# Performance work log

Measured on AMD Instinct MI355X. Metric: run time of the kernel, lower is better.

Reference implementation:

```python
import jax, jax.numpy as jnp
import numpy as np

MAX_LV = 2
N_NODES = 20000
N_CLASSES = 16


def setup_inputs() -> dict:
    key = jax.random.key(0)
    ks = jax.random.split(key, 20)
    B, E, A, F, D, H, NI = 8, 320000, 512, 128, 64, 64, 16
    s = 0.05
    return {
        "node_features": jax.random.normal(ks[0], (N_NODES, F), jnp.float32) * s,
        "w_n2l": jax.random.normal(ks[1], (F, D), jnp.float32) * s,
        "bias_n2l": jax.random.normal(ks[2], (D,), jnp.float32) * s,
        "conv_w": jax.random.normal(ks[3], (D, D), jnp.float32) * s,
        "conv_b": jax.random.normal(ks[4], (D,), jnp.float32) * s,
        "lin1_w": jax.random.normal(ks[5], (3 * D, H), jnp.float32) * s,
        "lin1_b": jax.random.normal(ks[6], (H,), jnp.float32) * s,
        "linout_w": jax.random.normal(ks[7], (H, 1), jnp.float32) * s,
        "linout_b": jax.random.normal(ks[8], (1,), jnp.float32) * s,
        "le1_w": jax.random.normal(ks[9], (N_CLASSES * NI, H), jnp.float32) * s,
        "le1_b": jax.random.normal(ks[10], (H,), jnp.float32) * s,
        "le2_w": jax.random.normal(ks[11], (H, D), jnp.float32) * s,
        "le2_b": jax.random.normal(ks[12], (D,), jnp.float32) * s,
        "edge_w": jax.random.uniform(ks[13], (B, E), jnp.float32),
        "rows": jax.random.randint(ks[14], (B, E), 0, N_NODES, jnp.int32),
        "cols": jax.random.randint(ks[15], (B, E), 0, N_NODES, jnp.int32),
        "labels": jax.random.randint(ks[16], (B, NI), 0, N_CLASSES, jnp.int32),
        "actions": jax.random.randint(ks[17], (B, A), 0, N_NODES, jnp.int32),
    }


def reference(node_features, w_n2l, bias_n2l, conv_w, conv_b,
              lin1_w, lin1_b, linout_w, linout_b,
              le1_w, le1_b, le2_w, le2_b,
              edge_w, rows, cols, labels, actions):
    B = edge_w.shape[0]
    D = w_n2l.shape[1]
    A = actions.shape[1]

    # shared node-embed base (torch: mm(node_features, w_n2l) + bias)
    input_message = node_features @ w_n2l + bias_n2l            # [N, D]
    h0 = jax.nn.relu(input_message)

    # per-graph spmm message passing: out[r] += w * h[c] for edge (r, c)
    def message_pass(r, c, ew):
        h = h0
        for _ in range(MAX_LV):
            n2npool = jax.ops.segment_sum(ew[:, None] * h[c], r,
                                          num_segments=N_NODES)   # [N, D]
            h = jax.nn.relu(n2npool @ conv_w + conv_b + input_message)
        return h

    h = jax.vmap(message_pass)(rows, cols, edge_w)               # [B, N, D]
    graph_embed = jnp.mean(h, axis=1)                            # [B, D]

    # label embedding: one-hot(labels) flattened -> two relu linears
    onehot = jax.nn.one_hot(labels, N_CLASSES,
                            dtype=h.dtype).reshape(B, -1)        # [B, C*NI]
    x = jax.nn.relu(onehot @ le1_w + le1_b)
    label_embed = jax.nn.relu(x @ le2_w + le2_b)                 # [B, D]

    # gather candidate action embeddings (time_t != 2 branch)
    action_embed = jnp.take_along_axis(
        h, actions[:, :, None].astype(jnp.int32), axis=1)        # [B, A, D]

    embed_s = jnp.concatenate([graph_embed, label_embed], axis=-1)  # [B, 2D]
    embed_s_a = jnp.concatenate(
        [jnp.broadcast_to(embed_s[:, None, :], (B, A, 2 * D)), action_embed],
        axis=-1)                                                 # [B, A, 3D]

    z = jax.nn.relu(embed_s_a @ lin1_w + lin1_b)                 # [B, A, H]
    raw_pred = (z @ linout_w + linout_b)[..., 0]                 # [B, A]
    preds = jnp.max(raw_pred, axis=1)                            # [B]
    return preds
```

## Files before the change

kernel.cpp:

```cpp
#include <hip/hip_runtime.h>
#include <hip/hip_bf16.h>

#define N_NODES 20000
#define F_DIM 128
#define D_DIM 64
#define B_GR 8
#define E_EDGES 320000
#define A_ACT 512
#define NI_L 16
#define NCLS 16
#define NBUK 160
#define RPB  125
#define CAP  6144

typedef __hip_bfloat16 bf16;
typedef __attribute__((ext_vector_type(8))) short bf16x8;
typedef __attribute__((ext_vector_type(4))) float f32x4;

static __device__ __forceinline__ short f2bf(float x) {
    __hip_bfloat16 h = __float2bfloat16(x);
    return *reinterpret_cast<short*>(&h);
}

__global__ __launch_bounds__(256) void k_n2l(const float* __restrict__ nf,
        const float* __restrict__ w, const float* __restrict__ bias,
        const float* __restrict__ convb,
        float* __restrict__ imb, bf16* __restrict__ h0b) {
    __shared__ float Wl[F_DIM * D_DIM];
    for (int i = threadIdx.x; i < F_DIM * D_DIM; i += 256) Wl[i] = w[i];
    __syncthreads();
    int lane = threadIdx.x & 63;
    int wid = (blockIdx.x * 256 + threadIdx.x) >> 6;
    int nw  = (gridDim.x * 256) >> 6;
    float b = bias[lane];
    float cb = convb[lane];
    for (int n = wid; n < N_NODES; n += nw) {
        const float* nfr = nf + (size_t)n * F_DIM;
        float acc = b;
        #pragma unroll 8
        for (int k = 0; k < F_DIM; ++k)
            acc = fmaf(nfr[k], Wl[k * D_DIM + lane], acc);
        imb[n * D_DIM + lane] = acc + cb;
        h0b[n * D_DIM + lane] = __float2bfloat16(fmaxf(acc, 0.f));
    }
}

__global__ __launch_bounds__(256) void k_bcnt(const int* __restrict__ rows,
        int* __restrict__ bcnt) {
    __shared__ int lcnt[NBUK];
    for (int i = threadIdx.x; i < NBUK; i += 256) lcnt[i] = 0;
    __syncthreads();
    int g = blockIdx.x & 7;
    int chunk = blockIdx.x >> 3;
    int nb = gridDim.x >> 3;
    int per = (E_EDGES + nb - 1) / nb;
    int e0 = chunk * per, e1 = min(e0 + per, E_EDGES);
    const int* rg = rows + (size_t)g * E_EDGES;
    for (int e = e0 + (int)threadIdx.x; e < e1; e += 256)
        atomicAdd(&lcnt[rg[e] / RPB], 1);
    __syncthreads();
    for (int i = threadIdx.x; i < NBUK; i += 256)
        if (lcnt[i]) atomicAdd(&bcnt[g * NBUK + i], lcnt[i]);
}

__global__ __launch_bounds__(256) void k_bscan(const int* __restrict__ bcnt,
        int* __restrict__ bptr, int* __restrict__ bcur) {
    int g = blockIdx.x;
    __shared__ int part[256];
    int t = threadIdx.x;
    int v = (t < NBUK) ? bcnt[g * NBUK + t] : 0;
    part[t] = v;
    __syncthreads();
    for (int off = 1; off < 256; off <<= 1) {
        int u = (t >= off) ? part[t - off] : 0;
        __syncthreads();
        part[t] += u;
        __syncthreads();
    }
    int excl = part[t] - v;
    if (t <= NBUK) bptr[g * (NBUK + 1) + t] = excl;
    if (t < NBUK)  bcur[g * NBUK + t] = excl;
}

__global__ __launch_bounds__(256) void k_part(const int* __restrict__ rows,
        const int* __restrict__ cols, const float* __restrict__ ew,
        int* __restrict__ bcur, float2* __restrict__ temp) {
    int g = blockIdx.x & 7;
    int chunk = blockIdx.x >> 3;
    int nb = gridDim.x >> 3;
    int per = (E_EDGES + nb - 1) / nb;
    int e0 = chunk * per, e1 = min(e0 + per, E_EDGES);
    const int*   rg = rows + (size_t)g * E_EDGES;
    const int*   cg = cols + (size_t)g * E_EDGES;
    const float* wg = ew   + (size_t)g * E_EDGES;
    float2* tg = temp + (size_t)g * E_EDGES;
    __shared__ int lcnt[NBUK];
    __shared__ int lbase[NBUK];
    for (int base = e0; base < e1; base += 1024) {
        for (int i = threadIdx.x; i < NBUK; i += 256) lcnt[i] = 0;
        __syncthreads();
        int r[4], c[4], bk[4], rk[4]; float w[4];
        #pragma unroll
        for (int j = 0; j < 4; ++j) {
            int e = base + (int)threadIdx.x + j * 256;
            if (e < e1) {
                r[j] = rg[e]; c[j] = cg[e]; w[j] = wg[e];
                bk[j] = r[j] / RPB;
                rk[j] = atomicAdd(&lcnt[bk[j]], 1);
            } else bk[j] = -1;
        }
        __syncthreads();
        for (int i = threadIdx.x; i < NBUK; i += 256)
            if (lcnt[i]) lbase[i] = atomicAdd(&bcur[g * NBUK + i], lcnt[i]);
        __syncthreads();
        #pragma unroll
        for (int j = 0; j < 4; ++j)
            if (bk[j] >= 0)
                tg[lbase[bk[j]] + rk[j]] =
                    make_float2(__int_as_float((r[j] << 15) | c[j]), w[j]);
        __syncthreads();
    }
}

__global__ __launch_bounds__(256) void k_scat3(const float2* __restrict__ temp,
        const int* __restrict__ bptr, int* __restrict__ ptr,
        float2* __restrict__ cw) {
    __shared__ int hist[RPB];
    __shared__ int curs[RPB];
    __shared__ int part[128];
    __shared__ float2 buf[CAP];
    int t = threadIdx.x;
    int g = blockIdx.x & 7;
    int b = blockIdx.x >> 3;
    int row0 = b * RPB;
    int e0 = bptr[g * (NBUK + 1) + b];
    int e1 = bptr[g * (NBUK + 1) + b + 1];
    int sz = e1 - e0;
    const float2* tg = temp + (size_t)g * E_EDGES;
    float2* cwg = cw + (size_t)g * E_EDGES;

    for (int i = t; i < RPB; i += 256) hist[i] = 0;
    __syncthreads();
    for (int e = e0 + t; e < e1; e += 256) {
        unsigned u = (unsigned)__float_as_int(tg[e].x);
        atomicAdd(&hist[(int)(u >> 15) - row0], 1);
    }
    __syncthreads();
    if (t < 128) part[t] = (t < RPB) ? hist[t] : 0;
    __syncthreads();
    for (int off = 1; off < 128; off <<= 1) {
        int v = (t < 128 && t >= off) ? part[t - off] : 0;
        __syncthreads();
        if (t < 128) part[t] += v;
        __syncthreads();
    }
    if (t < RPB) {
        int excl = part[t] - hist[t];
        ptr[g * (N_NODES + 1) + row0 + t] = e0 + excl;
        curs[t] = excl;
    }
    if (b == NBUK - 1 && t == 0) ptr[g * (N_NODES + 1) + N_NODES] = e1;
    __syncthreads();

    if (sz <= CAP) {
        for (int e = e0 + t; e < e1; e += 256) {
            float2 d = tg[e];
            unsigned u = (unsigned)__float_as_int(d.x);
            int pos = atomicAdd(&curs[(int)(u >> 15) - row0], 1);
            buf[pos] = make_float2(__int_as_float((int)(u & 32767u)), d.y);
        }
        __syncthreads();
        for (int i = t; i < sz; i += 256) cwg[e0 + i] = buf[i];
    } else {
        for (int e = e0 + t; e < e1; e += 256) {
            float2 d = tg[e];
            unsigned u = (unsigned)__float_as_int(d.x);
            int pos = atomicAdd(&curs[(int)(u >> 15) - row0], 1);
            cwg[e0 + pos] = make_float2(__int_as_float((int)(u & 32767u)), d.y);
        }
    }
}

template <int NGR>
__global__ __launch_bounds__(256) void k_gemm(const bf16* __restrict__ src,
        const float* __restrict__ convw, bf16* __restrict__ dst) {
    __shared__ __align__(16) short Wt[64 * 64];
    __shared__ __align__(16) float Cl[4][16 * 68];
    for (int i = threadIdx.x; i < 4096; i += 256) {
        int n = i >> 6, k = i & 63;
        Wt[(n << 6) | k] = f2bf(convw[(k << 6) | n]);
    }
    __syncthreads();
    int lane = threadIdx.x & 63;
    int wv   = threadIdx.x >> 6;
    int r    = lane & 15;
    int kg   = lane >> 4;
    bf16x8 Bf[4][2];
    #pragma unroll
    for (int t = 0; t < 4; ++t)
        #pragma unroll
        for (int s = 0; s < 2; ++s)
            Bf[t][s] = *(const bf16x8*)&Wt[(((t << 4) + r) << 6) + (s << 5) + (kg << 3)];

    int g = blockIdx.x & (NGR - 1);
    int chunk = blockIdx.x / NGR;
    int n0 = ((chunk << 2) + wv) << 4;
    if (n0 >= N_NODES) return;
    const bf16* sg = src + (size_t)g * N_NODES * D_DIM;
    bf16* dg = dst + (size_t)g * N_NODES * D_DIM;
    float* Cw = Cl[wv];

    f32x4 c0 = {0,0,0,0}, c1 = {0,0,0,0}, c2 = {0,0,0,0}, c3 = {0,0,0,0};
    #pragma unroll
    for (int s = 0; s < 2; ++s) {
        bf16x8 a = *(const bf16x8*)&sg[((n0 + r) << 6) + (s << 5) + (kg << 3)];
        c0 = __builtin_amdgcn_mfma_f32_16x16x32_bf16(a, Bf[0][s], c0, 0, 0, 0);
        c1 = __builtin_amdgcn_mfma_f32_16x16x32_bf16(a, Bf[1][s], c1, 0, 0, 0);
        c2 = __builtin_amdgcn_mfma_f32_16x16x32_bf16(a, Bf[2][s], c2, 0, 0, 0);
        c3 = __builtin_amdgcn_mfma_f32_16x16x32_bf16(a, Bf[3][s], c3, 0, 0, 0);
    }
    #pragma unroll
    for (int q = 0; q < 4; ++q) {
        Cw[((kg << 2) + q) * 68 +  0 + r] = c0[q];
        Cw[((kg << 2) + q) * 68 + 16 + r] = c1[q];
        Cw[((kg << 2) + q) * 68 + 32 + r] = c2[q];
        Cw[((kg << 2) + q) * 68 + 48 + r] = c3[q];
    }
    #pragma unroll
    for (int i = 0; i < 16; ++i)
        dg[((n0 + i) << 6) | lane] = __float2bfloat16(Cw[i * 68 + lane]);
}

template <bool DO_GE, bool STORE_H>
__global__ __launch_bounds__(256) void k_gather(const bf16* __restrict__ hW,
        size_t src_stride, const int* __restrict__ ptr,
        const float2* __restrict__ cw, const float* __restrict__ imb,
        bf16* __restrict__ hout, float* __restrict__ ge) {
    int lane = threadIdx.x & 63;
    int wv   = threadIdx.x >> 6;
    int g    = blockIdx.x & 7;
    int chunk = blockIdx.x >> 3;
    const int CH = gridDim.x >> 3;
    int waves_per_graph = CH * 4;
    int npw = (N_NODES + waves_per_graph - 1) / waves_per_graph;
    int n0 = (chunk * 4 + wv) * npw;
    int n1 = min(n0 + npw, N_NODES);
    if (n0 >= n1) return;

    const bf16*   sg  = hW + (size_t)g * src_stride;
    const int*    pg  = ptr + g * (N_NODES + 1);
    const float2* cwg = cw + (size_t)g * E_EDGES;
    bf16* hg = hout + (size_t)g * N_NODES * D_DIM;
    float gsum = 0.f;

    int s0 = pg[n0];
    for (int n = n0; n < n1; ++n) {
        int s1 = pg[n + 1];
        float imv = imb[(n << 6) | lane];
        float a0 = 0.f, a1 = 0.f, a2 = 0.f, a3 = 0.f;
        int e = s0;
        for (; e + 8 <= s1; e += 8) {
            float2 c0 = cwg[e],   c1 = cwg[e+1], c2 = cwg[e+2], c3 = cwg[e+3];
            float2 c4 = cwg[e+4], c5 = cwg[e+5], c6 = cwg[e+6], c7 = cwg[e+7];
            float v0 = __bfloat162float(sg[((size_t)__float_as_int(c0.x) << 6) | lane]);
            float v1 = __bfloat162float(sg[((size_t)__float_as_int(c1.x) << 6) | lane]);
            float v2 = __bfloat162float(sg[((size_t)__float_as_int(c2.x) << 6) | lane]);
            float v3 = __bfloat162float(sg[((size_t)__float_as_int(c3.x) << 6) | lane]);
            float v4 = __bfloat162float(sg[((size_t)__float_as_int(c4.x) << 6) | lane]);
            float v5 = __bfloat162float(sg[((size_t)__float_as_int(c5.x) << 6) | lane]);
            float v6 = __bfloat162float(sg[((size_t)__float_as_int(c6.x) << 6) | lane]);
            float v7 = __bfloat162float(sg[((size_t)__float_as_int(c7.x) << 6) | lane]);
            a0 = fmaf(v0, c0.y, a0); a1 = fmaf(v1, c1.y, a1);
            a2 = fmaf(v2, c2.y, a2); a3 = fmaf(v3, c3.y, a3);
            a0 = fmaf(v4, c4.y, a0); a1 = fmaf(v5, c5.y, a1);
            a2 = fmaf(v6, c6.y, a2); a3 = fmaf(v7, c7.y, a3);
        }
        for (; e + 2 <= s1; e += 2) {
            float2 c0 = cwg[e], c1 = cwg[e+1];
            float v0 = __bfloat162float(sg[((size_t)__float_as_int(c0.x) << 6) | lane]);
            float v1 = __bfloat162float(sg[((size_t)__float_as_int(c1.x) << 6) | lane]);
            a0 = fmaf(v0, c0.y, a0); a1 = fmaf(v1, c1.y, a1);
        }
        if (e < s1) {
            float2 cv = cwg[e];
            float v = __bfloat162float(sg[((size_t)__float_as_int(cv.x) << 6) | lane]);
            a2 = fmaf(v, cv.y, a2);
        }
        s0 = s1;
        float hv = ((a0 + a1) + (a2 + a3)) + imv;
        hv = fmaxf(hv, 0.f);
        if (STORE_H) hg[((size_t)n << 6) | lane] = __float2bfloat16(hv);
        gsum += hv;
    }
    if (DO_GE) atomicAdd(&ge[g * D_DIM + lane], gsum);
}

__global__ __launch_bounds__(256) void k_act(const bf16* __restrict__ hW,
        const int* __restrict__ ptr, const float2* __restrict__ cw,
        const float* __restrict__ imb, const int* __restrict__ actions,
        float* __restrict__ act_emb) {
    int lane = threadIdx.x & 63;
    int wv   = threadIdx.x >> 6;
    int g    = blockIdx.x & 7;
    int a    = (blockIdx.x >> 3) * 4 + wv;
    int node = actions[(size_t)g * A_ACT + a];

    const bf16*   sg  = hW + (size_t)g * N_NODES * D_DIM;
    const int*    pg  = ptr + g * (N_NODES + 1);
    const float2* cwg = cw + (size_t)g * E_EDGES;
    int s0 = pg[node], s1 = pg[node + 1];
    float acc = 0.f;
    for (int e = s0; e < s1; ++e) {
        float2 cv = cwg[e];
        float v = __bfloat162float(sg[((size_t)__float_as_int(cv.x) << 6) | lane]);
        acc = fmaf(v, cv.y, acc);
    }
    float hv = fmaxf(acc + imb[(node << 6) | lane], 0.f);
    act_emb[((size_t)g * A_ACT + a) * D_DIM + lane] = hv;
}

__global__ __launch_bounds__(512) void k_small(const int* __restrict__ labels,
        const float* __restrict__ le1w, const float* __restrict__ le1b,
        const float* __restrict__ le2w, const float* __restrict__ le2b,
        float* __restrict__ ge, float* __restrict__ le) {
    int b = threadIdx.x >> 6;
    int lane = threadIdx.x & 63;
    ge[b * D_DIM + lane] *= (1.f / (float)N_NODES);
    float x = le1b[lane];
    #pragma unroll
    for (int i = 0; i < NI_L; ++i) {
        int cls = labels[b * NI_L + i];
        x += le1w[(i * NCLS + cls) * D_DIM + lane];
    }
    x = fmaxf(x, 0.f);
    float acc = le2b[lane];
    for (int hh = 0; hh < D_DIM; ++hh)
        acc = fmaf(__shfl(x, hh), le2w[hh * D_DIM + lane], acc);
    le[b * D_DIM + lane] = fmaxf(acc, 0.f);
}

__global__ __launch_bounds__(256) void k_tail(const float* __restrict__ ge,
        const float* __restrict__ le, const float* __restrict__ act_emb,
        const float* __restrict__ lin1w, const float* __restrict__ lin1b,
        const float* __restrict__ loutw, const float* __restrict__ loutb,
        float* __restrict__ raw) {
    __shared__ float Wl[192 * 64];
    for (int i = threadIdx.x; i < 192 * 64; i += 256) Wl[i] = lin1w[i];
    __syncthreads();
    int lane = threadIdx.x & 63;
    int wv = blockIdx.x * 4 + (threadIdx.x >> 6);
    if (wv >= B_GR * A_ACT) return;
    int b = wv >> 9;
    float e2 = act_emb[(size_t)wv * D_DIM + lane];
    const float* geb = ge + b * D_DIM;
    const float* leb = le + b * D_DIM;
    float z = lin1b[lane];
    #pragma unroll 4
    for (int k = 0; k < 64; ++k) z = fmaf(geb[k], Wl[k * 64 + lane], z);
    #pragma unroll 4
    for (int k = 0; k < 64; ++k) z = fmaf(leb[k], Wl[(64 + k) * 64 + lane], z);
    #pragma unroll 4
    for (int k = 0; k < 64; ++k) z = fmaf(__shfl(e2, k), Wl[(128 + k) * 64 + lane], z);
    z = fmaxf(z, 0.f);
    float r = z * loutw[lane];
    #pragma unroll
    for (int off = 32; off; off >>= 1) r += __shfl_xor(r, off);
    if (lane == 0) raw[wv] = r + loutb[0];
}

__global__ __launch_bounds__(512) void k_max(const float* __restrict__ raw,
        float* __restrict__ out) {
    int b = threadIdx.x >> 6, lane = threadIdx.x & 63;
    float m = -INFINITY;
    for (int a = lane; a < A_ACT; a += 64) m = fmaxf(m, raw[b * A_ACT + a]);
    #pragma unroll
    for (int off = 32; off; off >>= 1) m = fmaxf(m, __shfl_xor(m, off));
    if (lane == 0) out[b] = m;
}

extern "C" void kernel_launch(void* const* d_in, const int* in_sizes, int n_in,
                              void* d_out, int out_size, void* d_ws, size_t ws_size,
                              hipStream_t stream) {
    const float* nf      = (const float*)d_in[0];
    const float* w_n2l   = (const float*)d_in[1];
    const float* bias_n2l= (const float*)d_in[2];
    const float* conv_w  = (const float*)d_in[3];
    const float* conv_b  = (const float*)d_in[4];
    const float* lin1_w  = (const float*)d_in[5];
    const float* lin1_b  = (const float*)d_in[6];
    const float* linout_w= (const float*)d_in[7];
    const float* linout_b= (const float*)d_in[8];
    const float* le1_w   = (const float*)d_in[9];
    const float* le1_b   = (const float*)d_in[10];
    const float* le2_w   = (const float*)d_in[11];
    const float* le2_b   = (const float*)d_in[12];
    const float* edge_w  = (const float*)d_in[13];
    const int*   rows    = (const int*)d_in[14];
    const int*   cols    = (const int*)d_in[15];
    const int*   labels  = (const int*)d_in[16];
    const int*   actions = (const int*)d_in[17];
    float* out = (float*)d_out;

    const size_t NE = (size_t)N_NODES * D_DIM;

    float2* cw  = (float2*)d_ws;
    bf16*  h1   = (bf16*)(cw + (size_t)B_GR * E_EDGES);
    float2* temp = (float2*)h1;
    bf16*  hW1  = h1 + 8 * NE;
    float* imb  = (float*)(hW1 + 8 * NE);
    bf16*  h0b  = (bf16*)(imb + NE);
    bf16*  hW0  = h0b + NE;
    float* act  = (float*)(hW0 + NE);
    float* ge   = act + (size_t)B_GR * A_ACT * D_DIM;
    float* le   = ge + 512;
    float* raw  = le + 512;
    int*   bcnt = (int*)(raw + B_GR * A_ACT);
    int*   bptr = bcnt + B_GR * NBUK;
    int*   bcur = bptr + B_GR * (NBUK + 1);
    int*   ptr  = bcur + B_GR * NBUK;

    k_n2l<<<512, 256, 0, stream>>>(nf, w_n2l, bias_n2l, conv_b, imb, h0b);
    hipMemsetAsync(bcnt, 0, (size_t)B_GR * NBUK * sizeof(int), stream);
    hipMemsetAsync(ge, 0, 512 * sizeof(float), stream);

    k_bcnt<<<1024, 256, 0, stream>>>(rows, bcnt);
    k_bscan<<<B_GR, 256, 0, stream>>>(bcnt, bptr, bcur);

    k_gemm<1><<<313, 256, 0, stream>>>(h0b, conv_w, hW0);

    k_part<<<1024, 256, 0, stream>>>(rows, cols, edge_w, bcur, temp);
    k_scat3<<<NBUK * 8, 256, 0, stream>>>(temp, bptr, ptr, cw);

    k_gather<false, true><<<512 * 8, 256, 0, stream>>>(
            hW0, 0, ptr, cw, imb, h1, nullptr);

    k_gemm<8><<<313 * 8, 256, 0, stream>>>(h1, conv_w, hW1);

    k_gather<true, false><<<512 * 8, 256, 0, stream>>>(
            hW1, NE, ptr, cw, imb, nullptr, ge);

    k_act<<<(A_ACT / 4) * 8, 256, 0, stream>>>(hW1, ptr, cw, imb, actions, act);

    k_small<<<1, 512, 0, stream>>>(labels, le1_w, le1_b, le2_w, le2_b, ge, le);
    k_tail<<<(B_GR * A_ACT) / 4, 256, 0, stream>>>(ge, le, act, lin1_w, lin1_b,
                                                   linout_w, linout_b, raw);
    k_max<<<1, 512, 0, stream>>>(raw, out);
}
```

Measured before the change: 323.2 us.

## Process four edges per wave with 16-lane groups loading 8-byte bf16 chunks

The CSR gather kernel now splits each 64-lane wave into four 16-lane groups. Each group handles a different edge and loads four bf16 features per lane as one 8-byte load, so a wave covers four edges per load instead of one. Partial sums are combined across groups with xor shuffles, and one group adds the bias, applies relu and writes packed bf16 output. The aim is more memory-level parallelism and fewer, wider load instructions, at the cost of shuffle overhead, idle lanes in the epilogue and masked tail work for low-degree nodes.

```diff
diff --git a/kernel.cpp b/kernel.cpp
--- a/kernel.cpp
+++ b/kernel.cpp
@@ -20,6 +20,9 @@
 static __device__ __forceinline__ short f2bf(float x) {
     __hip_bfloat16 h = __float2bfloat16(x);
     return *reinterpret_cast<short*>(&h);
+}
+static __device__ __forceinline__ unsigned f2bfu(float x) {
+    return (unsigned short)f2bf(x);
 }
 
 __global__ __launch_bounds__(256) void k_n2l(const float* __restrict__ nf,
@@ -237,6 +240,8 @@
         const float2* __restrict__ cw, const float* __restrict__ imb,
         bf16* __restrict__ hout, float* __restrict__ ge) {
     int lane = threadIdx.x & 63;
+    int grp  = lane >> 4;
+    int sub  = lane & 15;
     int wv   = threadIdx.x >> 6;
     int g    = blockIdx.x & 7;
     int chunk = blockIdx.x >> 3;
@@ -251,48 +256,74 @@
     const int*    pg  = ptr + g * (N_NODES + 1);
     const float2* cwg = cw + (size_t)g * E_EDGES;
     bf16* hg = hout + (size_t)g * N_NODES * D_DIM;
-    float gsum = 0.f;
+    float gs0 = 0.f, gs1 = 0.f, gs2 = 0.f, gs3 = 0.f;
 
     int s0 = pg[n0];
     for (int n = n0; n < n1; ++n) {
         int s1 = pg[n + 1];
-        float imv = imb[(n << 6) | lane];
-        float a0 = 0.f, a1 = 0.f, a2 = 0.f, a3 = 0.f;
+        float x0=0.f,x1=0.f,x2=0.f,x3=0.f, y0=0.f,y1=0.f,y2=0.f,y3=0.f;
         int e = s0;
         for (; e + 8 <= s1; e += 8) {
-            float2 c0 = cwg[e],   c1 = cwg[e+1], c2 = cwg[e+2], c3 = cwg[e+3];
-            float2 c4 = cwg[e+4], c5 = cwg[e+5], c6 = cwg[e+6], c7 = cwg[e+7];
-            float v0 = __bfloat162float(sg[((size_t)__float_as_int(c0.x) << 6) | lane]);
-            float v1 = __bfloat162float(sg[((size_t)__float_as_int(c1.x) << 6) | lane]);
-            float v2 = __bfloat162float(sg[((size_t)__float_as_int(c2.x) << 6) | lane]);
-            float v3 = __bfloat162float(sg[((size_t)__float_as_int(c3.x) << 6) | lane]);
-            float v4 = __bfloat162float(sg[((size_t)__float_as_int(c4.x) << 6) | lane]);
-            float v5 = __bfloat162float(sg[((size_t)__float_as_int(c5.x) << 6) | lane]);
-            float v6 = __bfloat162float(sg[((size_t)__float_as_int(c6.x) << 6) | lane]);
-            float v7 = __bfloat162float(sg[((size_t)__float_as_int(c7.x) << 6) | lane]);
-            a0 = fmaf(v0, c0.y, a0); a1 = fmaf(v1, c1.y, a1);
-            a2 = fmaf(v2, c2.y, a2); a3 = fmaf(v3, c3.y, a3);
-            a0 = fmaf(v4, c4.y, a0); a1 = fmaf(v5, c5.y, a1);
-            a2 = fmaf(v6, c6.y, a2); a3 = fmaf(v7, c7.y, a3);
-        }
-        for (; e + 2 <= s1; e += 2) {
-            float2 c0 = cwg[e], c1 = cwg[e+1];
-            float v0 = __bfloat162float(sg[((size_t)__float_as_int(c0.x) << 6) | lane]);
-            float v1 = __bfloat162float(sg[((size_t)__float_as_int(c1.x) << 6) | lane]);
-            a0 = fmaf(v0, c0.y, a0); a1 = fmaf(v1, c1.y, a1);
-        }
-        if (e < s1) {
-            float2 cv = cwg[e];
-            float v = __bfloat162float(sg[((size_t)__float_as_int(cv.x) << 6) | lane]);
-            a2 = fmaf(v, cv.y, a2);
+            float2 ca = cwg[e + grp];
+            float2 cb = cwg[e + 4 + grp];
+            uint2 da = *(const uint2*)&sg[((size_t)__float_as_int(ca.x) << 6) + (sub << 2)];
+            uint2 db = *(const uint2*)&sg[((size_t)__float_as_int(cb.x) << 6) + (sub << 2)];
+            float wa = ca.y, wb = cb.y;
+            x0 = fmaf(__int_as_float((int)(da.x << 16)), wa, x0);
+            x1 = fmaf(__int_as_float((int)(da.x & 0xffff0000u)), wa, x1);
+            x2 = fmaf(__int_as_float((int)(da.y << 16)), wa, x2);
+            x3 = fmaf(__int_as_float((int)(da.y & 0xffff0000u)), wa, x3);
+            y0 = fmaf(__int_as_float((int)(db.x << 16)), wb, y0);
+            y1 = fmaf(__int_as_float((int)(db.x & 0xffff0000u)), wb, y1);
+            y2 = fmaf(__int_as_float((int)(db.y << 16)), wb, y2);
+            y3 = fmaf(__int_as_float((int)(db.y & 0xffff0000u)), wb, y3);
+        }
+        int rem = s1 - e;
+        if (rem > 0) {
+            float2 ca = cwg[min(e + grp, s1 - 1)];
+            float wa = (grp < rem) ? ca.y : 0.f;
+            uint2 da = *(const uint2*)&sg[((size_t)__float_as_int(ca.x) << 6) + (sub << 2)];
+            x0 = fmaf(__int_as_float((int)(da.x << 16)), wa, x0);
+            x1 = fmaf(__int_as_float((int)(da.x & 0xffff0000u)), wa, x1);
+            x2 = fmaf(__int_as_float((int)(da.y << 16)), wa, x2);
+            x3 = fmaf(__int_as_float((int)(da.y & 0xffff0000u)), wa, x3);
+            if (rem > 4) {
+                float2 cb = cwg[min(e + 4 + grp, s1 - 1)];
+                float wb = (grp + 4 < rem) ? cb.y : 0.f;
+                uint2 db = *(const uint2*)&sg[((size_t)__float_as_int(cb.x) << 6) + (sub << 2)];
+                y0 = fmaf(__int_as_float((int)(db.x << 16)), wb, y0);
+                y1 = fmaf(__int_as_float((int)(db.x & 0xffff0000u)), wb, y1);
+                y2 = fmaf(__int_as_float((int)(db.y << 16)), wb, y2);
+                y3 = fmaf(__int_as_float((int)(db.y & 0xffff0000u)), wb, y3);
+            }
         }
         s0 = s1;
-        float hv = ((a0 + a1) + (a2 + a3)) + imv;
-        hv = fmaxf(hv, 0.f);
-        if (STORE_H) hg[((size_t)n << 6) | lane] = __float2bfloat16(hv);
-        gsum += hv;
-    }
-    if (DO_GE) atomicAdd(&ge[g * D_DIM + lane], gsum);
+        x0 += y0; x1 += y1; x2 += y2; x3 += y3;
+        x0 += __shfl_xor(x0, 16); x0 += __shfl_xor(x0, 32);
+        x1 += __shfl_xor(x1, 16); x1 += __shfl_xor(x1, 32);
+        x2 += __shfl_xor(x2, 16); x2 += __shfl_xor(x2, 32);
+        x3 += __shfl_xor(x3, 16); x3 += __shfl_xor(x3, 32);
+        if (grp == 0) {
+            const float4 iv = *(const float4*)&imb[(n << 6) + (sub << 2)];
+            float h0 = fmaxf(x0 + iv.x, 0.f);
+            float h1 = fmaxf(x1 + iv.y, 0.f);
+            float h2 = fmaxf(x2 + iv.z, 0.f);
+            float h3 = fmaxf(x3 + iv.w, 0.f);
+            if (STORE_H) {
+                uint2 o;
+                o.x = (f2bfu(h1) << 16) | f2bfu(h0);
+                o.y = (f2bfu(h3) << 16) | f2bfu(h2);
+                *(uint2*)&hg[((size_t)n << 6) + (sub << 2)] = o;
+            }
+            gs0 += h0; gs1 += h1; gs2 += h2; gs3 += h3;
+        }
+    }
+    if (DO_GE && grp == 0) {
+        atomicAdd(&ge[g * D_DIM + (sub << 2) + 0], gs0);
+        atomicAdd(&ge[g * D_DIM + (sub << 2) + 1], gs1);
+        atomicAdd(&ge[g * D_DIM + (sub << 2) + 2], gs2);
+        atomicAdd(&ge[g * D_DIM + (sub << 2) + 3], gs3);
+    }
 }
 
 __global__ __launch_bounds__(256) void k_act(const bf16* __restrict__ hW,
```

After: 451.4 us. 39.7% more time.
